# Kernel optimization log

Measured on AMD Instinct MI355X. Metric: run time of the kernel, lower is better.

Reference implementation:

```python
import jax, jax.numpy as jnp
import numpy as np

R = 16            # search_range
D = 2 * R + 1     # 33 offsets per axis -> 1089 cost channels
B, C, H, W = 64, 256, 16, 16
OUT = 512         # conv channels for search_range=16
FULLY = 1024
EPS_BN = 1e-5
EPS_NORM = 1e-12
LRELU_SLOPE = 0.01


def l2_normalize(x):
    # torch F.normalize(x, dim=1, p=2): x / clamp_min(||x||_2, 1e-12)
    n = jnp.sqrt(jnp.sum(x * x, axis=1, keepdims=True))
    return x / jnp.maximum(n, EPS_NORM)


def cost_volume(c1, warp, r):
    # Fused equivalent of the original (2r+1)^2 Python-loop of slice/mul/mean:
    # one dense correlation GEMM over the padded map, then a gather of the
    # diagonal-band entries. cost[b,dy,dx,i,j] = mean_c c1[b,c,i,j]*pad[b,c,i+dy,j+dx]
    b, c, h, w = c1.shape
    d = 2 * r + 1
    padded = jnp.pad(warp, ((0, 0), (0, 0), (r, r), (r, r)))          # (B,C,h+2r,w+2r)
    full = jnp.einsum('bcij,bcuv->bijuv', c1, padded) / c             # (B,h,w,h+2r,w+2r)
    dy = jnp.arange(d)
    ii = jnp.arange(h)
    jj = jnp.arange(w)
    I = ii[None, None, :, None]                 # (1,1,h,1)
    J = jj[None, None, None, :]                 # (1,1,1,w)
    U = dy[:, None, None, None] + I             # (d,1,h,1)
    V = dy[None, :, None, None] + J             # (1,d,1,w)
    cost = full[:, I, J, U, V]                  # (B,d,d,h,w)
    cost = cost.reshape(b, d * d, h, w)
    return jnp.where(cost > 0, cost, LRELU_SLOPE * cost)  # LeakyReLU(0.01)


def conv_bn_relu(x, Wc, bc, g, be, stride):
    y = jax.lax.conv_general_dilated(
        x, Wc, window_strides=(stride, stride), padding=((1, 1), (1, 1)),
        dimension_numbers=('NCHW', 'OIHW', 'NCHW'))
    y = y + bc[None, :, None, None]
    # training-mode BatchNorm: biased batch stats over (B,H,W)
    mu = jnp.mean(y, axis=(0, 2, 3), keepdims=True)
    var = jnp.var(y, axis=(0, 2, 3), keepdims=True)
    y = (y - mu) * jax.lax.rsqrt(var + EPS_BN)
    y = y * g[None, :, None, None] + be[None, :, None, None]
    return jnp.maximum(y, 0.0)


def setup_inputs() -> dict:
    key = jax.random.key(0)
    ks = jax.random.split(key, 10)
    s = 0.02
    inp = {
        'feature1': jax.random.normal(ks[0], (B, C, H, W), jnp.float32),
        'feature2': jax.random.normal(ks[1], (B, C, H, W), jnp.float32),
        'W1': jax.random.normal(ks[2], (OUT, D * D, 3, 3), jnp.float32) * s,
        'b1': jnp.zeros((OUT,), jnp.float32),
        'g1': jnp.ones((OUT,), jnp.float32),
        'be1': jnp.zeros((OUT,), jnp.float32),
        'W2': jax.random.normal(ks[3], (OUT, OUT, 3, 3), jnp.float32) * s,
        'b2': jnp.zeros((OUT,), jnp.float32),
        'g2': jnp.ones((OUT,), jnp.float32),
        'be2': jnp.zeros((OUT,), jnp.float32),
        'W3': jax.random.normal(ks[4], (OUT, OUT, 3, 3), jnp.float32) * s,
        'b3': jnp.zeros((OUT,), jnp.float32),
        'g3': jnp.ones((OUT,), jnp.float32),
        'be3': jnp.zeros((OUT,), jnp.float32),
        'Wf1': jax.random.normal(ks[5], (FULLY, 256 * OUT), jnp.float32) * s,
        'bf1': jnp.zeros((FULLY,), jnp.float32),
        'Wf2': jax.random.normal(ks[6], (8, FULLY), jnp.float32) * s,
        'bf2': jnp.zeros((8,), jnp.float32),
    }
    return inp


def reference(feature1, feature2, W1, b1, g1, be1, W2, b2, g2, be2,
              W3, b3, g3, be3, Wf1, bf1, Wf2, bf2):
    # warped=False: normalize both feature maps
    gc = cost_volume(l2_normalize(feature1), l2_normalize(feature2), R)
    x = conv_bn_relu(gc, W1, b1, g1, be1, 1)
    x = conv_bn_relu(x, W2, b2, g2, be2, 1)
    x = conv_bn_relu(x, W3, b3, g3, be3, 1)
    x = x.reshape(x.shape[0], -1)               # (B, 512*16*16)
    x = jnp.maximum(x @ Wf1.T + bf1, 0.0)       # Linear + ReLU
    # Dropout treated as identity (deterministic reference)
    offset = x @ Wf2.T + bf2                    # (B, 8)
    return offset
```

## Files before the change

### kernel.cpp

```cpp
#include <hip/hip_runtime.h>
#include <hip/hip_bf16.h>
#include <stdint.h>


typedef unsigned short ushort_t;
typedef __attribute__((ext_vector_type(8))) short     bf16x8;
typedef __attribute__((ext_vector_type(8))) unsigned short u16x8;
typedef __attribute__((ext_vector_type(4))) unsigned short u16x4;
typedef __attribute__((ext_vector_type(4))) float     f32x4;

#define NB   64
#define NC   256
#define NP   256
#define KCV  256
#define KP1  1152
#define NOUT 512
#define NROWS 16384
#define KFC  131072
#define NF   1024
#define KSPL 32

__device__ __forceinline__ unsigned short f2bf(float x) {
  union { float f; unsigned u; } c; c.f = x;
  unsigned r = c.u + 0x7FFFu + ((c.u >> 16) & 1u);
// ... 89 lines not shown
                  : (const ushort_t*)0;
  }

  for (int kc = 0; kc < KCV; kc += 64) {
#pragma unroll
    for (int s = 0; s < 4; ++s) {
      int idx = tid + (s << 8);
      gl_lds16(srcA[s] + kc, &As[idx * 8]);
      const ushort_t* g = srcB[s] ? srcB[s] + kc : zerot;
      gl_lds16(g, &Bs[idx * 8]);
    }
    __syncthreads();
#pragma unroll
    for (int kk = 0; kk < 2; ++kk) {
      bf16x8 af[4], bfv[4];
#pragma unroll
      for (int mi = 0; mi < 4; ++mi)
        af[mi] = *(const bf16x8*)&As[(wr * 64 + mi * 16 + la) * 64 + kk * 32 + lb * 8];
#pragma unroll
      for (int ni = 0; ni < 4; ++ni)
        bfv[ni] = *(const bf16x8*)&Bs[(wc * 64 + ni * 16 + la) * 64 + kk * 32 + lb * 8];
#pragma unroll
      for (int mi = 0; mi < 4; ++mi)
#pragma unroll
        for (int ni = 0; ni < 4; ++ni)
          acc[mi][ni] = mfma16(af[mi], bfv[ni], acc[mi][ni]);
    }
    __syncthreads();
  }

  const float sc = 1.f / 256.f;
#pragma unroll
  for (int ni = 0; ni < 4; ++ni) {
    int uv = n0 + wc * 64 + ni * 16 + la;
    int u = uv / 48, v = uv - u * 48;
#pragma unroll
    for (int mi = 0; mi < 4; ++mi) {
      int ij = m0 + wr * 64 + mi * 16 + lb * 4;
#pragma unroll
      for (int r = 0; r < 4; ++r) {
        int ijr = ij + r;
        int i = ijr >> 4, j = ijr & 15;
        int dy = u - i, dx = v - j;
        if ((unsigned)dy < 33u && (unsigned)dx < 33u) {
          float vv = acc[mi][ni][r] * sc;
          vv = vv > 0.f ? vv : 0.01f * vv;
          costT[((size_t)b * NP + ijr) * KP1 + dy * 33 + dx] = f2bf(vv);
        }
      }
    }
  }
}

__global__ __launch_bounds__(512, 1) void conv_gemm256(
    const ushort_t* __restrict__ X, const ushort_t* __restrict__ Wp,
    const float* __restrict__ bias, ushort_t* __restrict__ Y0,
    ushort_t* __restrict__ Y1, const int K, const int TPT, const int NT2,
    const ushort_t* __restrict__ zerot)
{
  __shared__ ushort_t lds[65536];
  const int tid = threadIdx.x;
  const int lane = tid & 63, wave = tid >> 6;
  const int wr = wave >> 2, wc = wave & 3;
  const int la = lane & 15, lb = lane >> 4;

  const int bid = blockIdx.x;
  const int L = ((bid & 7) << 5) + (bid >> 3);
  const int g = L >> 7;
  const int rem = L & 127;
  const int b = rem >> 1;
  const int n0 = (rem & 1) << 8;
  const int t0 = g * NT2;

  int amask[4];
  const ushort_t* abase[4];
  const ushort_t* bbase[4];
#pragma unroll
  for (int s = 0; s < 4; ++s) {
    int idx = tid + (s << 9);
    int ks = idx & 7, loc = (idx >> 3) & 63;
    int rA = ((s & 1) << 7) + ((s >> 1) << 6) + loc;
    int i = rA >> 4, j = rA & 15;
    int m = 0;
#pragma unroll
    for (int tap = 0; tap < 9; ++tap) {
      int i2 = i + tap / 3 - 1, j2 = j + tap % 3 - 1;
      if (((unsigned)i2 < 16u) & ((unsigned)j2 < 16u)) m |= 1 << tap;
    }
    amask[s] = m;
    abase[s] = X + (size_t)(b * NP + rA) * K + ((ks ^ (rA & 7)) << 3);
    int rB = ((s & 1) << 7) + ((loc >> 5) << 6) + ((s >> 1) << 5) + (loc & 31);
    bbase[s] = Wp + (size_t)(n0 + rB) * K + ((ks ^ (rB & 7)) << 3);
  }

  const int ck0 = ((0 + lb) ^ (la & 7)) << 3;
  const int ck1 = ((4 + lb) ^ (la & 7)) << 3;
  const int a_base = wr * 4096 + la * 64;
  const int b_base = 16384 + (wc >> 1) * 4096 + (wc & 1) * 2048 + la * 64;

  f32x4 acc[8][4];
#pragma unroll
  for (int i = 0; i < 8; ++i)
#pragma unroll
    for (int j = 0; j < 4; ++j) acc[i][j] = (f32x4){0.f, 0.f, 0.f, 0.f};

  auto tile_par = [&](int tg, int& toffA, size_t& wtap, int& tap) {
    tap = tg / TPT;
    int kc = (tg - tap * TPT) << 6;
    int ty = tap / 3;
    toffA = (ty * 16 + (tap - 3 * ty) - 17) * K + kc;
    wtap  = (size_t)tap * NOUT * K + kc;
  };

#define STAGE_A(S) { const ushort_t* gp = ((amask[S] >> tapN) & 1) ? abase[S] + toffN : zerot; \
                     gl_lds16(gp, &bufn[(tid + ((S) << 9)) * 8]); }
#define STAGE_B(S) gl_lds16(bbase[S] + wtapN, &bufn[16384 + (tid + ((S) << 9)) * 8]);

#define READ_A03() \
  Af[0][0] = *(const bf16x8*)&buf[a_base + 0    + ck0]; Af[0][1] = *(const bf16x8*)&buf[a_base + 0    + ck1]; \
  Af[1][0] = *(const bf16x8*)&buf[a_base + 1024 + ck0]; Af[1][1] = *(const bf16x8*)&buf[a_base + 1024 + ck1]; \
  Af[2][0] = *(const bf16x8*)&buf[a_base + 2048 + ck0]; Af[2][1] = *(const bf16x8*)&buf[a_base + 2048 + ck1]; \
  Af[3][0] = *(const bf16x8*)&buf[a_base + 3072 + ck0]; Af[3][1] = *(const bf16x8*)&buf[a_base + 3072 + ck1];
#define READ_A47() \
  Af[4][0] = *(const bf16x8*)&buf[a_base + 8192 + 0    + ck0]; Af[4][1] = *(const bf16x8*)&buf[a_base + 8192 + 0    + ck1]; \
  Af[5][0] = *(const bf16x8*)&buf[a_base + 8192 + 1024 + ck0]; Af[5][1] = *(const bf16x8*)&buf[a_base + 8192 + 1024 + ck1]; \
  Af[6][0] = *(const bf16x8*)&buf[a_base + 8192 + 2048 + ck0]; Af[6][1] = *(const bf16x8*)&buf[a_base + 8192 + 2048 + ck1]; \
  Af[7][0] = *(const bf16x8*)&buf[a_base + 8192 + 3072 + ck0]; Af[7][1] = *(const bf16x8*)&buf[a_base + 8192 + 3072 + ck1];
#define READ_B(NOFF) \
  bf00 = *(const bf16x8*)&buf[b_base + (NOFF) + 0    + ck0]; bf01 = *(const bf16x8*)&buf[b_base + (NOFF) + 0    + ck1]; \
  bf10 = *(const bf16x8*)&buf[b_base + (NOFF) + 1024 + ck0]; bf11 = *(const bf16x8*)&buf[b_base + (NOFF) + 1024 + ck1];
#define MFMA_QUAD(MB, N0, N1) \
  acc[MB+0][N0] = mfma16(Af[MB+0][0], bf00, acc[MB+0][N0]); \
  acc[MB+0][N1] = mfma16(Af[MB+0][0], bf10, acc[MB+0][N1]); \
  acc[MB+1][N0] = mfma16(Af[MB+1][0], bf00, acc[MB+1][N0]); \
  acc[MB+1][N1] = mfma16(Af[MB+1][0], bf10, acc[MB+1][N1]); \
  acc[MB+2][N0] = mfma16(Af[MB+2][0], bf00, acc[MB+2][N0]); \
  acc[MB+2][N1] = mfma16(Af[MB+2][0], bf10, acc[MB+2][N1]); \
  acc[MB+3][N0] = mfma16(Af[MB+3][0], bf00, acc[MB+3][N0]); \
  acc[MB+3][N1] = mfma16(Af[MB+3][0], bf10, acc[MB+3][N1]); \
  acc[MB+0][N0] = mfma16(Af[MB+0][1], bf01, acc[MB+0][N0]); \
  acc[MB+0][N1] = mfma16(Af[MB+0][1], bf11, acc[MB+0][N1]); \
  acc[MB+1][N0] = mfma16(Af[MB+1][1], bf01, acc[MB+1][N0]); \
  acc[MB+1][N1] = mfma16(Af[MB+1][1], bf11, acc[MB+1][N1]); \
  acc[MB+2][N0] = mfma16(Af[MB+2][1], bf01, acc[MB+2][N0]); \
  acc[MB+2][N1] = mfma16(Af[MB+2][1], bf11, acc[MB+2][N1]); \
  acc[MB+3][N0] = mfma16(Af[MB+3][1], bf01, acc[MB+3][N0]); \
  acc[MB+3][N1] = mfma16(Af[MB+3][1], bf11, acc[MB+3][N1]);

  {
    ushort_t* bufn = &lds[0];
    int tapN, toffN; size_t wtapN;
    tile_par(t0, toffN, wtapN, tapN);
    STAGE_A(0) STAGE_A(1) STAGE_A(2) STAGE_A(3)
    STAGE_B(0) STAGE_B(1) STAGE_B(2) STAGE_B(3)
  }
  asm volatile("s_waitcnt vmcnt(2)" ::: "memory");
  __builtin_amdgcn_s_barrier();

  bf16x8 Af[8][2];

  for (int t = 0; t < NT2 - 1; ++t) {
    const ushort_t* buf = &lds[(t & 1) << 15];
    ushort_t* bufn = &lds[((t + 1) & 1) << 15];
    int tapN, toffN; size_t wtapN;
    tile_par(t0 + t + 1, toffN, wtapN, tapN);
    bf16x8 bf00, bf01, bf10, bf11;

    READ_A03()
    READ_B(0)
    STAGE_A(0) STAGE_A(1)
    asm volatile("s_waitcnt vmcnt(6)" ::: "memory");
    __builtin_amdgcn_s_barrier();
    asm volatile("s_waitcnt lgkmcnt(0)" ::: "memory");
    __builtin_amdgcn_sched_barrier(0);
    __builtin_amdgcn_s_setprio(1);
    MFMA_QUAD(0, 0, 1)
    __builtin_amdgcn_s_setprio(0);

    READ_A47()
    READ_B(0)
    STAGE_A(2) STAGE_A(3)
    asm volatile("s_waitcnt vmcnt(4)" ::: "memory");
    __builtin_amdgcn_s_barrier();
    asm volatile("s_waitcnt lgkmcnt(0)" ::: "memory");
    __builtin_amdgcn_sched_barrier(0);
    __builtin_amdgcn_s_setprio(1);
    MFMA_QUAD(4, 0, 1)
    __builtin_amdgcn_s_setprio(0);

    READ_B(8192)
    STAGE_B(0) STAGE_B(1)
    __builtin_amdgcn_s_barrier();
    asm volatile("s_waitcnt lgkmcnt(0)" ::: "memory");
    __builtin_amdgcn_sched_barrier(0);
    __builtin_amdgcn_s_setprio(1);
    MFMA_QUAD(0, 2, 3)
    __builtin_amdgcn_s_setprio(0);

    READ_B(8192)
    STAGE_B(2) STAGE_B(3)
    asm volatile("s_waitcnt vmcnt(2)" ::: "memory");
    __builtin_amdgcn_s_barrier();
    asm volatile("s_waitcnt lgkmcnt(0)" ::: "memory");
    __builtin_amdgcn_sched_barrier(0);
    __builtin_amdgcn_s_setprio(1);
    MFMA_QUAD(4, 2, 3)
    __builtin_amdgcn_s_setprio(0);
  }

  {
    const ushort_t* buf = &lds[((NT2 - 1) & 1) << 15];
    bf16x8 bf00, bf01, bf10, bf11;
    asm volatile("s_waitcnt vmcnt(0)" ::: "memory");
    __builtin_amdgcn_s_barrier();
    READ_A03()
    READ_B(0)
    asm volatile("s_waitcnt lgkmcnt(0)" ::: "memory");
    __builtin_amdgcn_sched_barrier(0);
    MFMA_QUAD(0, 0, 1)
    READ_A47()
    asm volatile("s_waitcnt lgkmcnt(0)" ::: "memory");
    __builtin_amdgcn_sched_barrier(0);
    MFMA_QUAD(4, 0, 1)
    READ_B(8192)
    asm volatile("s_waitcnt lgkmcnt(0)" ::: "memory");
    __builtin_amdgcn_sched_barrier(0);
    MFMA_QUAD(0, 2, 3)
    MFMA_QUAD(4, 2, 3)
  }

  ushort_t* Yh = g ? Y1 : Y0;
#pragma unroll
  for (int ni = 0; ni < 4; ++ni) {
    int col = n0 + wc * 64 + ni * 16 + la;
    float bv = 0.5f * bias[col];
#pragma unroll
    for (int mi = 0; mi < 8; ++mi) {
      int row = b * NP + wr * 128 + mi * 16 + lb * 4;
#pragma unroll
      for (int r = 0; r < 4; ++r)
        Yh[(size_t)(row + r) * NOUT + col] = f2bf(acc[mi][ni][r] + bv);
    }
  }
#undef STAGE_A
#undef STAGE_B
#undef READ_A03
#undef READ_A47
#undef READ_B
#undef MFMA_QUAD
}

__global__ __launch_bounds__(512) void bn_stat2(
    const ushort_t* __restrict__ Y0, const ushort_t* __restrict__ Y1,
    float* __restrict__ st)
{
  const int col = threadIdx.x;
  const size_t base = (size_t)blockIdx.x * 32 * NOUT;
  float s = 0.f, q = 0.f;
  for (int r = 0; r < 32; ++r) {
    float y = b2f(Y0[base + r * NOUT + col]) + b2f(Y1[base + r * NOUT + col]);
    s += y; q += y * y;
  }
  atomicAdd(&st[col], s);
  atomicAdd(&st[512 + col], q);
}

__global__ __launch_bounds__(256) void bn_apply2(
    const ushort_t* __restrict__ Y0, const ushort_t* __restrict__ Y1,
    const float* __restrict__ st, const float* __restrict__ g,
    const float* __restrict__ be, ushort_t* __restrict__ Xo)
{
  const size_t idx = (size_t)blockIdx.x * 256 + threadIdx.x;
  u16x8 a = *(const u16x8*)(Y0 + idx * 8);
  u16x8 c = *(const u16x8*)(Y1 + idx * 8);
  const int c0 = (int)((idx * 8) & 511);
  u16x8 pk;
#pragma unroll
  for (int q = 0; q < 8; ++q) {
    int cc = c0 + q;
    float y = b2f(a[q]) + b2f(c[q]);
    float mu  = st[cc] * (1.f / 16384.f);
    float var = st[512 + cc] * (1.f / 16384.f) - mu * mu;
    float s = rsqrtf(var + 1e-5f) * g[cc];
    pk[q] = f2bf(fmaxf((y - mu) * s + be[cc], 0.f));
  }
  *(u16x8*)(Xo + idx * 8) = pk;
}

__global__ __launch_bounds__(256) void bn_apply2_t(
    const ushort_t* __restrict__ Y0, const ushort_t* __restrict__ Y1,
    const float* __restrict__ st, const float* __restrict__ g,
    const float* __restrict__ be, ushort_t* __restrict__ Xf)
{
  __shared__ ushort_t T[64][65];
  const int c0  = blockIdx.x * 64;
  const int ij0 = blockIdx.y * 64;
  const int b   = blockIdx.z;
  const int tid = threadIdx.x;

#pragma unroll
  for (int it = 0; it < 16; ++it) {
    int e = it * 256 + tid;
// ... 127 lines not shown
  const float* g2  = (const float*)d_in[8];
  const float* be2 = (const float*)d_in[9];
  const float* W3  = (const float*)d_in[10];
  const float* b3  = (const float*)d_in[11];
  const float* g3  = (const float*)d_in[12];
  const float* be3 = (const float*)d_in[13];
  const float* Wf1 = (const float*)d_in[14];
  const float* bf1 = (const float*)d_in[15];
  const float* Wf2 = (const float*)d_in[16];
  const float* bf2 = (const float*)d_in[17];
  float* out = (float*)d_out;

  char* ws = (char*)d_ws;
  size_t off = 0;
  auto alloc = [&](size_t bytes) -> void* {
    void* p = ws + off;
    off += (bytes + 255) & ~(size_t)255;
    return p;
  };

  ushort_t* zerot = (ushort_t*)alloc(256);
  float* st1  = (float*)alloc(1024 * 4);
  float* st2  = (float*)alloc(1024 * 4);
  float* st3  = (float*)alloc(1024 * 4);
  const size_t zero_bytes = off;

  float* hacc = (float*)alloc((size_t)KSPL * NB * NF * 4);
  const size_t SZ_AT   = (size_t)NB * NP * NC * 2;
  const size_t SZ_COST = (size_t)NB * NP * KP1 * 2;
  const size_t SZ_WP1  = (size_t)9 * NOUT * KP1 * 2;
  const size_t SZ_WP23 = (size_t)9 * NOUT * 512 * 2;
  ushort_t* AT    = (ushort_t*)alloc(SZ_AT);
  ushort_t* N2T   = (ushort_t*)alloc(SZ_AT);
  ushort_t* costT = (ushort_t*)alloc(SZ_COST);
  ushort_t* Wp1   = (ushort_t*)alloc(SZ_WP1);
  ushort_t* Wp2   = (ushort_t*)alloc(SZ_WP23);
  ushort_t* Wp3   = (ushort_t*)alloc(SZ_WP23);
  ushort_t* Yh0   = (ushort_t*)alloc((size_t)NROWS * NOUT * 2);
  ushort_t* Yh1   = (ushort_t*)alloc((size_t)NROWS * NOUT * 2);
  ushort_t* Xbuf  = (ushort_t*)alloc((size_t)NROWS * NOUT * 2);
  ushort_t* Xf    = (ushort_t*)alloc((size_t)NB * KFC * 2);

  hipMemsetAsync(ws, 0, zero_bytes, stream);
  hipMemsetAsync(costT, 0, SZ_COST, stream);

  l2norm_t<<<dim3(64, 2), 256, 0, stream>>>(f1, f2, AT, N2T);

  pack_w<<<(9 * NOUT * KP1 + 255) / 256, 256, 0, stream>>>(W1, Wp1, 1089, KP1, 9 * NOUT * KP1);
  pack_w<<<(9 * NOUT * 512 + 255) / 256, 256, 0, stream>>>(W2, Wp2, 512, 512, 9 * NOUT * 512);
  pack_w<<<(9 * NOUT * 512 + 255) / 256, 256, 0, stream>>>(W3, Wp3, 512, 512, 9 * NOUT * 512);

  cv_gemm<<<dim3(18, 2, 64), 256, 0, stream>>>(AT, N2T, costT, zerot);

  conv_gemm256<<<256, 512, 0, stream>>>(costT, Wp1, b1, Yh0, Yh1, KP1, 18, 81, zerot);
  bn_stat2<<<512, 512, 0, stream>>>(Yh0, Yh1, st1);
  bn_apply2<<<4096, 256, 0, stream>>>(Yh0, Yh1, st1, g1, be1, Xbuf);

  conv_gemm256<<<256, 512, 0, stream>>>(Xbuf, Wp2, b2, Yh0, Yh1, 512, 8, 36, zerot);
  bn_stat2<<<512, 512, 0, stream>>>(Yh0, Yh1, st2);
  bn_apply2<<<4096, 256, 0, stream>>>(Yh0, Yh1, st2, g2, be2, Xbuf);

  conv_gemm256<<<256, 512, 0, stream>>>(Xbuf, Wp3, b3, Yh0, Yh1, 512, 8, 36, zerot);
  bn_stat2<<<512, 512, 0, stream>>>(Yh0, Yh1, st3);
  bn_apply2_t<<<dim3(8, 4, 64), 256, 0, stream>>>(Yh0, Yh1, st3, g3, be3, Xf);

  fc1_gemm<<<dim3(16, KSPL), 256, 0, stream>>>(Xf, Wf1, hacc);
  fc2_out<<<64, 256, 0, stream>>>(hacc, bf1, Wf2, bf2, out);

  (void)in_sizes; (void)n_in; (void)out_size; (void)ws_size;
}
```

Before: 621.2 us.

## Reuse staged activation tile across all nine conv taps via shifted LDS reads

The implicit-GEMM conv kernel now loads each 256-row by 64-channel activation chunk into LDS once and reuses it for all nine 3x3 taps. It does this by reading LDS rows shifted by the tap offset, with out-of-bounds rows redirected to a zeroed LDS slot. Before, a masked, shifted copy of the activations was re-fetched from global memory for every tap. The aim is to cut global and L2 traffic for the A operand roughly ninefold. In exchange the weight tile is still streamed every tap, with only double buffering, and the schedule waits with vmcnt(0) after each tap, which may expose load latency.

```diff
diff --git a/kernel.cpp b/kernel.cpp
--- a/kernel.cpp
+++ b/kernel.cpp
@@ -165,13 +165,12 @@
   }
 }
 
-__global__ __launch_bounds__(512, 1) void conv_gemm256(
+__global__ __launch_bounds__(512, 1) void conv_tap(
     const ushort_t* __restrict__ X, const ushort_t* __restrict__ Wp,
     const float* __restrict__ bias, ushort_t* __restrict__ Y0,
-    ushort_t* __restrict__ Y1, const int K, const int TPT, const int NT2,
-    const ushort_t* __restrict__ zerot)
-{
-  __shared__ ushort_t lds[65536];
+    ushort_t* __restrict__ Y1, const int K, const int Kh, const int nc)
+{
+  __shared__ ushort_t lds[65600];
   const int tid = threadIdx.x;
   const int lane = tid & 63, wave = tid >> 6;
   const int wr = wave >> 2, wc = wave & 3;
@@ -183,33 +182,25 @@
   const int rem = L & 127;
   const int b = rem >> 1;
   const int n0 = (rem & 1) << 8;
-  const int t0 = g * NT2;
-
-  int amask[4];
+  const int koff0 = g * Kh;
+
+  if (tid < 8) *(u16x8*)&lds[65536 + tid * 8] = (u16x8){0,0,0,0,0,0,0,0};
+
   const ushort_t* abase[4];
   const ushort_t* bbase[4];
 #pragma unroll
   for (int s = 0; s < 4; ++s) {
     int idx = tid + (s << 9);
-    int ks = idx & 7, loc = (idx >> 3) & 63;
-    int rA = ((s & 1) << 7) + ((s >> 1) << 6) + loc;
-    int i = rA >> 4, j = rA & 15;
-    int m = 0;
-#pragma unroll
-    for (int tap = 0; tap < 9; ++tap) {
-      int i2 = i + tap / 3 - 1, j2 = j + tap % 3 - 1;
-      if (((unsigned)i2 < 16u) & ((unsigned)j2 < 16u)) m |= 1 << tap;
-    }
-    amask[s] = m;
-    abase[s] = X + (size_t)(b * NP + rA) * K + ((ks ^ (rA & 7)) << 3);
+    int row = idx >> 3, ck = idx & 7;
+    abase[s] = X + (size_t)(b * NP + row) * K + ((ck ^ (row & 7)) << 3);
+    int loc = (idx >> 3) & 63, ks = idx & 7;
     int rB = ((s & 1) << 7) + ((loc >> 5) << 6) + ((s >> 1) << 5) + (loc & 31);
     bbase[s] = Wp + (size_t)(n0 + rB) * K + ((ks ^ (rB & 7)) << 3);
   }
 
-  const int ck0 = ((0 + lb) ^ (la & 7)) << 3;
-  const int ck1 = ((4 + lb) ^ (la & 7)) << 3;
-  const int a_base = wr * 4096 + la * 64;
-  const int b_base = 16384 + (wc >> 1) * 4096 + (wc & 1) * 2048 + la * 64;
+  const int ckB0 = ((0 + lb) ^ (la & 7)) << 3;
+  const int ckB1 = ((4 + lb) ^ (la & 7)) << 3;
+  const int wread = (wc >> 1) * 4096 + (wc & 1) * 2048 + la * 64;
 
   f32x4 acc[8][4];
 #pragma unroll
@@ -217,129 +208,152 @@
 #pragma unroll
     for (int j = 0; j < 4; ++j) acc[i][j] = (f32x4){0.f, 0.f, 0.f, 0.f};
 
-  auto tile_par = [&](int tg, int& toffA, size_t& wtap, int& tap) {
-    tap = tg / TPT;
-    int kc = (tg - tap * TPT) << 6;
-    int ty = tap / 3;
-    toffA = (ty * 16 + (tap - 3 * ty) - 17) * K + kc;
-    wtap  = (size_t)tap * NOUT * K + kc;
-  };
-
-#define STAGE_A(S) { const ushort_t* gp = ((amask[S] >> tapN) & 1) ? abase[S] + toffN : zerot; \
-                     gl_lds16(gp, &bufn[(tid + ((S) << 9)) * 8]); }
-#define STAGE_B(S) gl_lds16(bbase[S] + wtapN, &bufn[16384 + (tid + ((S) << 9)) * 8]);
-
-#define READ_A03() \
-  Af[0][0] = *(const bf16x8*)&buf[a_base + 0    + ck0]; Af[0][1] = *(const bf16x8*)&buf[a_base + 0    + ck1]; \
-  Af[1][0] = *(const bf16x8*)&buf[a_base + 1024 + ck0]; Af[1][1] = *(const bf16x8*)&buf[a_base + 1024 + ck1]; \
-  Af[2][0] = *(const bf16x8*)&buf[a_base + 2048 + ck0]; Af[2][1] = *(const bf16x8*)&buf[a_base + 2048 + ck1]; \
-  Af[3][0] = *(const bf16x8*)&buf[a_base + 3072 + ck0]; Af[3][1] = *(const bf16x8*)&buf[a_base + 3072 + ck1];
-#define READ_A47() \
-  Af[4][0] = *(const bf16x8*)&buf[a_base + 8192 + 0    + ck0]; Af[4][1] = *(const bf16x8*)&buf[a_base + 8192 + 0    + ck1]; \
-  Af[5][0] = *(const bf16x8*)&buf[a_base + 8192 + 1024 + ck0]; Af[5][1] = *(const bf16x8*)&buf[a_base + 8192 + 1024 + ck1]; \
-  Af[6][0] = *(const bf16x8*)&buf[a_base + 8192 + 2048 + ck0]; Af[6][1] = *(const bf16x8*)&buf[a_base + 8192 + 2048 + ck1]; \
-  Af[7][0] = *(const bf16x8*)&buf[a_base + 8192 + 3072 + ck0]; Af[7][1] = *(const bf16x8*)&buf[a_base + 8192 + 3072 + ck1];
-#define READ_B(NOFF) \
-  bf00 = *(const bf16x8*)&buf[b_base + (NOFF) + 0    + ck0]; bf01 = *(const bf16x8*)&buf[b_base + (NOFF) + 0    + ck1]; \
-  bf10 = *(const bf16x8*)&buf[b_base + (NOFF) + 1024 + ck0]; bf11 = *(const bf16x8*)&buf[b_base + (NOFF) + 1024 + ck1];
-#define MFMA_QUAD(MB, N0, N1) \
-  acc[MB+0][N0] = mfma16(Af[MB+0][0], bf00, acc[MB+0][N0]); \
-  acc[MB+0][N1] = mfma16(Af[MB+0][0], bf10, acc[MB+0][N1]); \
-  acc[MB+1][N0] = mfma16(Af[MB+1][0], bf00, acc[MB+1][N0]); \
-  acc[MB+1][N1] = mfma16(Af[MB+1][0], bf10, acc[MB+1][N1]); \
-  acc[MB+2][N0] = mfma16(Af[MB+2][0], bf00, acc[MB+2][N0]); \
-  acc[MB+2][N1] = mfma16(Af[MB+2][0], bf10, acc[MB+2][N1]); \
-  acc[MB+3][N0] = mfma16(Af[MB+3][0], bf00, acc[MB+3][N0]); \
-  acc[MB+3][N1] = mfma16(Af[MB+3][0], bf10, acc[MB+3][N1]); \
-  acc[MB+0][N0] = mfma16(Af[MB+0][1], bf01, acc[MB+0][N0]); \
-  acc[MB+0][N1] = mfma16(Af[MB+0][1], bf11, acc[MB+0][N1]); \
-  acc[MB+1][N0] = mfma16(Af[MB+1][1], bf01, acc[MB+1][N0]); \
-  acc[MB+1][N1] = mfma16(Af[MB+1][1], bf11, acc[MB+1][N1]); \
-  acc[MB+2][N0] = mfma16(Af[MB+2][1], bf01, acc[MB+2][N0]); \
-  acc[MB+2][N1] = mfma16(Af[MB+2][1], bf11, acc[MB+2][N1]); \
-  acc[MB+3][N0] = mfma16(Af[MB+3][1], bf01, acc[MB+3][N0]); \
-  acc[MB+3][N1] = mfma16(Af[MB+3][1], bf11, acc[MB+3][N1]);
-
+  const int nsteps = nc * 9;
+
+#pragma unroll
+  for (int s = 0; s < 4; ++s)
+    gl_lds16(abase[s] + koff0, &lds[(tid + (s << 9)) * 8]);
   {
-    ushort_t* bufn = &lds[0];
-    int tapN, toffN; size_t wtapN;
-    tile_par(t0, toffN, wtapN, tapN);
-    STAGE_A(0) STAGE_A(1) STAGE_A(2) STAGE_A(3)
-    STAGE_B(0) STAGE_B(1) STAGE_B(2) STAGE_B(3)
-  }
-  asm volatile("s_waitcnt vmcnt(2)" ::: "memory");
+    size_t wko = (size_t)koff0;
+#pragma unroll
+    for (int s = 0; s < 4; ++s)
+      gl_lds16(bbase[s] + wko, &lds[32768 + (tid + (s << 9)) * 8]);
+  }
+  asm volatile("s_waitcnt vmcnt(0)" ::: "memory");
   __builtin_amdgcn_s_barrier();
 
-  bf16x8 Af[8][2];
-
-  for (int t = 0; t < NT2 - 1; ++t) {
-    const ushort_t* buf = &lds[(t & 1) << 15];
-    ushort_t* bufn = &lds[((t + 1) & 1) << 15];
-    int tapN, toffN; size_t wtapN;
-    tile_par(t0 + t + 1, toffN, wtapN, tapN);
-    bf16x8 bf00, bf01, bf10, bf11;
-
-    READ_A03()
-    READ_B(0)
-    STAGE_A(0) STAGE_A(1)
-    asm volatile("s_waitcnt vmcnt(6)" ::: "memory");
-    __builtin_amdgcn_s_barrier();
-    asm volatile("s_waitcnt lgkmcnt(0)" ::: "memory");
-    __builtin_amdgcn_sched_barrier(0);
-    __builtin_amdgcn_s_setprio(1);
-    MFMA_QUAD(0, 0, 1)
-    __builtin_amdgcn_s_setprio(0);
-
-    READ_A47()
-    READ_B(0)
-    STAGE_A(2) STAGE_A(3)
-    asm volatile("s_waitcnt vmcnt(4)" ::: "memory");
-    __builtin_amdgcn_s_barrier();
-    asm volatile("s_waitcnt lgkmcnt(0)" ::: "memory");
-    __builtin_amdgcn_sched_barrier(0);
-    __builtin_amdgcn_s_setprio(1);
-    MFMA_QUAD(4, 0, 1)
-    __builtin_amdgcn_s_setprio(0);
-
-    READ_B(8192)
-    STAGE_B(0) STAGE_B(1)
-    __builtin_amdgcn_s_barrier();
-    asm volatile("s_waitcnt lgkmcnt(0)" ::: "memory");
-    __builtin_amdgcn_sched_barrier(0);
-    __builtin_amdgcn_s_setprio(1);
-    MFMA_QUAD(0, 2, 3)
-    __builtin_amdgcn_s_setprio(0);
-
-    READ_B(8192)
-    STAGE_B(2) STAGE_B(3)
-    asm volatile("s_waitcnt vmcnt(2)" ::: "memory");
-    __builtin_amdgcn_s_barrier();
-    asm volatile("s_waitcnt lgkmcnt(0)" ::: "memory");
-    __builtin_amdgcn_sched_barrier(0);
-    __builtin_amdgcn_s_setprio(1);
-    MFMA_QUAD(4, 2, 3)
-    __builtin_amdgcn_s_setprio(0);
-  }
-
-  {
-    const ushort_t* buf = &lds[((NT2 - 1) & 1) << 15];
-    bf16x8 bf00, bf01, bf10, bf11;
-    asm volatile("s_waitcnt vmcnt(0)" ::: "memory");
-    __builtin_amdgcn_s_barrier();
-    READ_A03()
-    READ_B(0)
-    asm volatile("s_waitcnt lgkmcnt(0)" ::: "memory");
-    __builtin_amdgcn_sched_barrier(0);
-    MFMA_QUAD(0, 0, 1)
-    READ_A47()
-    asm volatile("s_waitcnt lgkmcnt(0)" ::: "memory");
-    __builtin_amdgcn_sched_barrier(0);
-    MFMA_QUAD(4, 0, 1)
-    READ_B(8192)
-    asm volatile("s_waitcnt lgkmcnt(0)" ::: "memory");
-    __builtin_amdgcn_sched_barrier(0);
-    MFMA_QUAD(0, 2, 3)
-    MFMA_QUAD(4, 2, 3)
+  for (int c = 0; c < nc; ++c) {
+    const int aC = (c & 1) << 14;
+    ushort_t* an = &lds[((c + 1) & 1) << 14];
+    for (int tap = 0; tap < 9; ++tap) {
+      const int step = c * 9 + tap;
+      const int wC = 32768 + ((step & 1) << 14);
+      ushort_t* wn = &lds[32768 + (((step + 1) & 1) << 14)];
+      const bool has_next = step < nsteps - 1;
+      const bool stageA = (tap == 7) && (c < nc - 1);
+      int tapN = (tap < 8) ? tap + 1 : 0;
+      int cN   = (tap < 8) ? c : c + 1;
+      size_t wkoN = (size_t)tapN * NOUT * K + koff0 + cN * 64;
+      int akoN = koff0 + (c + 1) * 64;
+
+      const int ty = tap / 3, tx = tap - 3 * ty;
+      const int dA = (ty - 1) * 16 + (tx - 1);
+      const int sx = (la + dA) & 7;
+      const int ckA0 = ((lb ^ sx) << 3);
+      const int ckA1 = (((4 + lb) ^ sx) << 3);
+      const int rbase = wr * 128 + la + dA;
+      const int ibase = wr * 8 + ty - 1;
+      const bool jok = !((tx == 0) & (la == 0)) & !((tx == 2) & (la == 15));
+
+      bf16x8 Af[4][2];
+      bf16x8 b01_00, b01_01, b01_10, b01_11;
+      bf16x8 b23_00, b23_01, b23_10, b23_11;
+
+#pragma unroll
+      for (int mi = 0; mi < 4; ++mi) {
+        bool ok = jok && ((unsigned)(ibase + mi) < 16u);
+        int r = (rbase + mi * 16) * 64;
+        int a0 = ok ? aC + r + ckA0 : 65536;
+        int a1 = ok ? aC + r + ckA1 : 65536;
+        Af[mi][0] = *(const bf16x8*)&lds[a0];
+        Af[mi][1] = *(const bf16x8*)&lds[a1];
+      }
+      b01_00 = *(const bf16x8*)&lds[wC + wread + 0    + ckB0];
+      b01_01 = *(const bf16x8*)&lds[wC + wread + 0    + ckB1];
+      b01_10 = *(const bf16x8*)&lds[wC + wread + 1024 + ckB0];
+      b01_11 = *(const bf16x8*)&lds[wC + wread + 1024 + ckB1];
+      if (has_next) {
+        gl_lds16(bbase[0] + wkoN, &wn[(tid + 0 * 512) * 8]);
+        gl_lds16(bbase[1] + wkoN, &wn[(tid + 1 * 512) * 8]);
+      }
+      asm volatile("s_waitcnt lgkmcnt(0)" ::: "memory");
+      __builtin_amdgcn_sched_barrier(0);
+      __builtin_amdgcn_s_setprio(1);
+#pragma unroll
+      for (int mi = 0; mi < 4; ++mi) {
+        acc[mi][0] = mfma16(Af[mi][0], b01_00, acc[mi][0]);
+        acc[mi][1] = mfma16(Af[mi][0], b01_10, acc[mi][1]);
+      }
+#pragma unroll
+      for (int mi = 0; mi < 4; ++mi) {
+        acc[mi][0] = mfma16(Af[mi][1], b01_01, acc[mi][0]);
+        acc[mi][1] = mfma16(Af[mi][1], b01_11, acc[mi][1]);
+      }
+      __builtin_amdgcn_s_setprio(0);
+
+      b23_00 = *(const bf16x8*)&lds[wC + 8192 + wread + 0    + ckB0];
+      b23_01 = *(const bf16x8*)&lds[wC + 8192 + wread + 0    + ckB1];
+      b23_10 = *(const bf16x8*)&lds[wC + 8192 + wread + 1024 + ckB0];
+      b23_11 = *(const bf16x8*)&lds[wC + 8192 + wread + 1024 + ckB1];
+      if (has_next) {
+        gl_lds16(bbase[2] + wkoN, &wn[(tid + 2 * 512) * 8]);
+        gl_lds16(bbase[3] + wkoN, &wn[(tid + 3 * 512) * 8]);
+      }
+      if (stageA) {
+        gl_lds16(abase[0] + akoN, &an[(tid + 0 * 512) * 8]);
+        gl_lds16(abase[1] + akoN, &an[(tid + 1 * 512) * 8]);
+      }
+      asm volatile("s_waitcnt lgkmcnt(0)" ::: "memory");
+      __builtin_amdgcn_sched_barrier(0);
+      __builtin_amdgcn_s_setprio(1);
+#pragma unroll
+      for (int mi = 0; mi < 4; ++mi) {
+        acc[mi][2] = mfma16(Af[mi][0], b23_00, acc[mi][2]);
+        acc[mi][3] = mfma16(Af[mi][0], b23_10, acc[mi][3]);
+      }
+#pragma unroll
+      for (int mi = 0; mi < 4; ++mi) {
+        acc[mi][2] = mfma16(Af[mi][1], b23_01, acc[mi][2]);
+        acc[mi][3] = mfma16(Af[mi][1], b23_11, acc[mi][3]);
+      }
+      __builtin_amdgcn_s_setprio(0);
+
+#pragma unroll
+      for (int mi = 0; mi < 4; ++mi) {
+        bool ok = jok && ((unsigned)(ibase + 4 + mi) < 16u);
+        int r = (rbase + (4 + mi) * 16) * 64;
+        int a0 = ok ? aC + r + ckA0 : 65536;
+        int a1 = ok ? aC + r + ckA1 : 65536;
+        Af[mi][0] = *(const bf16x8*)&lds[a0];
+        Af[mi][1] = *(const bf16x8*)&lds[a1];
+      }
+      if (stageA) {
+        gl_lds16(abase[2] + akoN, &an[(tid + 2 * 512) * 8]);
+        gl_lds16(abase[3] + akoN, &an[(tid + 3 * 512) * 8]);
+      }
+      asm volatile("s_waitcnt lgkmcnt(0)" ::: "memory");
+      __builtin_amdgcn_sched_barrier(0);
+      __builtin_amdgcn_s_setprio(1);
+#pragma unroll
+      for (int mi = 0; mi < 4; ++mi) {
+        acc[4 + mi][0] = mfma16(Af[mi][0], b01_00, acc[4 + mi][0]);
+        acc[4 + mi][1] = mfma16(Af[mi][0], b01_10, acc[4 + mi][1]);
+      }
+#pragma unroll
+      for (int mi = 0; mi < 4; ++mi) {
+        acc[4 + mi][0] = mfma16(Af[mi][1], b01_01, acc[4 + mi][0]);
+        acc[4 + mi][1] = mfma16(Af[mi][1], b01_11, acc[4 + mi][1]);
+      }
+      __builtin_amdgcn_s_setprio(0);
+
+      __builtin_amdgcn_s_setprio(1);
+#pragma unroll
+      for (int mi = 0; mi < 4; ++mi) {
+        acc[4 + mi][2] = mfma16(Af[mi][0], b23_00, acc[4 + mi][2]);
+        acc[4 + mi][3] = mfma16(Af[mi][0], b23_10, acc[4 + mi][3]);
+      }
+#pragma unroll
+      for (int mi = 0; mi < 4; ++mi) {
+        acc[4 + mi][2] = mfma16(Af[mi][1], b23_01, acc[4 + mi][2]);
+        acc[4 + mi][3] = mfma16(Af[mi][1], b23_11, acc[4 + mi][3]);
+      }
+      __builtin_amdgcn_s_setprio(0);
+      if (has_next) {
+        if (stageA) asm volatile("s_waitcnt vmcnt(4)" ::: "memory");
+        else        asm volatile("s_waitcnt vmcnt(0)" ::: "memory");
+      }
+      __builtin_amdgcn_s_barrier();
+    }
   }
 
   ushort_t* Yh = g ? Y1 : Y0;
@@ -355,12 +369,6 @@
         Yh[(size_t)(row + r) * NOUT + col] = f2bf(acc[mi][ni][r] + bv);
     }
   }
-#undef STAGE_A
-#undef STAGE_B
-#undef READ_A03
-#undef READ_A47
-#undef READ_B
-#undef MFMA_QUAD
 }
 
 __global__ __launch_bounds__(512) void bn_stat2(
@@ -594,15 +602,15 @@
 
   cv_gemm<<<dim3(18, 2, 64), 256, 0, stream>>>(AT, N2T, costT, zerot);
 
-  conv_gemm256<<<256, 512, 0, stream>>>(costT, Wp1, b1, Yh0, Yh1, KP1, 18, 81, zerot);
+  conv_tap<<<256, 512, 0, stream>>>(costT, Wp1, b1, Yh0, Yh1, KP1, 576, 9);
   bn_stat2<<<512, 512, 0, stream>>>(Yh0, Yh1, st1);
   bn_apply2<<<4096, 256, 0, stream>>>(Yh0, Yh1, st1, g1, be1, Xbuf);
 
-  conv_gemm256<<<256, 512, 0, stream>>>(Xbuf, Wp2, b2, Yh0, Yh1, 512, 8, 36, zerot);
+  conv_tap<<<256, 512, 0, stream>>>(Xbuf, Wp2, b2, Yh0, Yh1, 512, 256, 4);
   bn_stat2<<<512, 512, 0, stream>>>(Yh0, Yh1, st2);
   bn_apply2<<<4096, 256, 0, stream>>>(Yh0, Yh1, st2, g2, be2, Xbuf);
 
-  conv_gemm256<<<256, 512, 0, stream>>>(Xbuf, Wp3, b3, Yh0, Yh1, 512, 8, 36, zerot);
+  conv_tap<<<256, 512, 0, stream>>>(Xbuf, Wp3, b3, Yh0, Yh1, 512, 256, 4);
   bn_stat2<<<512, 512, 0, stream>>>(Yh0, Yh1, st3);
   bn_apply2_t<<<dim3(8, 4, 64), 256, 0, stream>>>(Yh0, Yh1, st3, g3, be3, Xf);
 
```

After: 622.1 us. Within noise of the previous version (+0.1%).

## Restructure conv GEMM into 8-phase ping-pong pipeline with channel-split K

Applied to the files above, without the earlier changes.

Rewrites the conv GEMM main loop into an 8-phase schedule that processes two K tiles per iteration. Each phase issues LDS reads plus part of the next tile's global-to-LDS staging, then runs 16 MFMAs between barriers. The split-K partition across the two output halves now divides the channel range instead of the flat tile range. Conv1 is padded to an even tile count, and out-of-range taps load from a zero tile. This adds extra barriers per phase and a full vmcnt(0) wait each half-iteration, which can stall the pipeline.

```diff
diff --git a/kernel.cpp b/kernel.cpp
--- a/kernel.cpp
+++ b/kernel.cpp
@@ -165,10 +165,10 @@
   }
 }
 
-__global__ __launch_bounds__(512, 1) void conv_gemm256(
+__global__ __launch_bounds__(512, 1) void conv8p(
     const ushort_t* __restrict__ X, const ushort_t* __restrict__ Wp,
     const float* __restrict__ bias, ushort_t* __restrict__ Y0,
-    ushort_t* __restrict__ Y1, const int K, const int TPT, const int NT2,
+    ushort_t* __restrict__ Y1, const int K, const int TPT, const int NT,
     const ushort_t* __restrict__ zerot)
 {
   __shared__ ushort_t lds[65536];
@@ -183,7 +183,7 @@
   const int rem = L & 127;
   const int b = rem >> 1;
   const int n0 = (rem & 1) << 8;
-  const int t0 = g * NT2;
+  const int koff0 = g * (TPT << 6);
 
   int amask[4];
   const ushort_t* abase[4];
@@ -191,9 +191,8 @@
 #pragma unroll
   for (int s = 0; s < 4; ++s) {
     int idx = tid + (s << 9);
-    int ks = idx & 7, loc = (idx >> 3) & 63;
-    int rA = ((s & 1) << 7) + ((s >> 1) << 6) + loc;
-    int i = rA >> 4, j = rA & 15;
+    int row = idx >> 3, ck = idx & 7;
+    int i = row >> 4, j = row & 15;
     int m = 0;
 #pragma unroll
     for (int tap = 0; tap < 9; ++tap) {
@@ -201,15 +200,14 @@
       if (((unsigned)i2 < 16u) & ((unsigned)j2 < 16u)) m |= 1 << tap;
     }
     amask[s] = m;
-    abase[s] = X + (size_t)(b * NP + rA) * K + ((ks ^ (rA & 7)) << 3);
-    int rB = ((s & 1) << 7) + ((loc >> 5) << 6) + ((s >> 1) << 5) + (loc & 31);
-    bbase[s] = Wp + (size_t)(n0 + rB) * K + ((ks ^ (rB & 7)) << 3);
-  }
-
-  const int ck0 = ((0 + lb) ^ (la & 7)) << 3;
-  const int ck1 = ((4 + lb) ^ (la & 7)) << 3;
-  const int a_base = wr * 4096 + la * 64;
-  const int b_base = 16384 + (wc >> 1) * 4096 + (wc & 1) * 2048 + la * 64;
+    abase[s] = X + (size_t)(b * NP + row) * K + ((ck ^ (row & 7)) << 3);
+    bbase[s] = Wp + (size_t)(n0 + row) * K + ((ck ^ (row & 7)) << 3);
+  }
+
+  const int ck0 = ((lb ^ (la & 7)) << 3);
+  const int ck1 = (((4 + lb) ^ (la & 7)) << 3);
+  const int arow = (wr * 128 + la) * 64;
+  const int brow = 16384 + (wc * 64 + la) * 64;
 
   f32x4 acc[8][4];
 #pragma unroll
@@ -217,129 +215,137 @@
 #pragma unroll
     for (int j = 0; j < 4; ++j) acc[i][j] = (f32x4){0.f, 0.f, 0.f, 0.f};
 
-  auto tile_par = [&](int tg, int& toffA, size_t& wtap, int& tap) {
-    tap = tg / TPT;
-    int kc = (tg - tap * TPT) << 6;
+  auto tpar = [&](int t, int& tap, int& toffA, size_t& wtap) {
+    tap = t / TPT;
+    int kc = koff0 + ((t - tap * TPT) << 6);
     int ty = tap / 3;
     toffA = (ty * 16 + (tap - 3 * ty) - 17) * K + kc;
     wtap  = (size_t)tap * NOUT * K + kc;
   };
 
-#define STAGE_A(S) { const ushort_t* gp = ((amask[S] >> tapN) & 1) ? abase[S] + toffN : zerot; \
-                     gl_lds16(gp, &bufn[(tid + ((S) << 9)) * 8]); }
-#define STAGE_B(S) gl_lds16(bbase[S] + wtapN, &bufn[16384 + (tid + ((S) << 9)) * 8]);
-
-#define READ_A03() \
-  Af[0][0] = *(const bf16x8*)&buf[a_base + 0    + ck0]; Af[0][1] = *(const bf16x8*)&buf[a_base + 0    + ck1]; \
-  Af[1][0] = *(const bf16x8*)&buf[a_base + 1024 + ck0]; Af[1][1] = *(const bf16x8*)&buf[a_base + 1024 + ck1]; \
-  Af[2][0] = *(const bf16x8*)&buf[a_base + 2048 + ck0]; Af[2][1] = *(const bf16x8*)&buf[a_base + 2048 + ck1]; \
-  Af[3][0] = *(const bf16x8*)&buf[a_base + 3072 + ck0]; Af[3][1] = *(const bf16x8*)&buf[a_base + 3072 + ck1];
-#define READ_A47() \
-  Af[4][0] = *(const bf16x8*)&buf[a_base + 8192 + 0    + ck0]; Af[4][1] = *(const bf16x8*)&buf[a_base + 8192 + 0    + ck1]; \
-  Af[5][0] = *(const bf16x8*)&buf[a_base + 8192 + 1024 + ck0]; Af[5][1] = *(const bf16x8*)&buf[a_base + 8192 + 1024 + ck1]; \
-  Af[6][0] = *(const bf16x8*)&buf[a_base + 8192 + 2048 + ck0]; Af[6][1] = *(const bf16x8*)&buf[a_base + 8192 + 2048 + ck1]; \
-  Af[7][0] = *(const bf16x8*)&buf[a_base + 8192 + 3072 + ck0]; Af[7][1] = *(const bf16x8*)&buf[a_base + 8192 + 3072 + ck1];
-#define READ_B(NOFF) \
-  bf00 = *(const bf16x8*)&buf[b_base + (NOFF) + 0    + ck0]; bf01 = *(const bf16x8*)&buf[b_base + (NOFF) + 0    + ck1]; \
-  bf10 = *(const bf16x8*)&buf[b_base + (NOFF) + 1024 + ck0]; bf11 = *(const bf16x8*)&buf[b_base + (NOFF) + 1024 + ck1];
-#define MFMA_QUAD(MB, N0, N1) \
-  acc[MB+0][N0] = mfma16(Af[MB+0][0], bf00, acc[MB+0][N0]); \
-  acc[MB+0][N1] = mfma16(Af[MB+0][0], bf10, acc[MB+0][N1]); \
-  acc[MB+1][N0] = mfma16(Af[MB+1][0], bf00, acc[MB+1][N0]); \
-  acc[MB+1][N1] = mfma16(Af[MB+1][0], bf10, acc[MB+1][N1]); \
-  acc[MB+2][N0] = mfma16(Af[MB+2][0], bf00, acc[MB+2][N0]); \
-  acc[MB+2][N1] = mfma16(Af[MB+2][0], bf10, acc[MB+2][N1]); \
-  acc[MB+3][N0] = mfma16(Af[MB+3][0], bf00, acc[MB+3][N0]); \
-  acc[MB+3][N1] = mfma16(Af[MB+3][0], bf10, acc[MB+3][N1]); \
-  acc[MB+0][N0] = mfma16(Af[MB+0][1], bf01, acc[MB+0][N0]); \
-  acc[MB+0][N1] = mfma16(Af[MB+0][1], bf11, acc[MB+0][N1]); \
-  acc[MB+1][N0] = mfma16(Af[MB+1][1], bf01, acc[MB+1][N0]); \
-  acc[MB+1][N1] = mfma16(Af[MB+1][1], bf11, acc[MB+1][N1]); \
-  acc[MB+2][N0] = mfma16(Af[MB+2][1], bf01, acc[MB+2][N0]); \
-  acc[MB+2][N1] = mfma16(Af[MB+2][1], bf11, acc[MB+2][N1]); \
-  acc[MB+3][N0] = mfma16(Af[MB+3][1], bf01, acc[MB+3][N0]); \
-  acc[MB+3][N1] = mfma16(Af[MB+3][1], bf11, acc[MB+3][N1]);
+#define STAGE_A(S, BUFN, TAPN, TOFFN) { \
+  const ushort_t* gp = ((amask[S] >> (TAPN)) & 1) ? abase[S] + (TOFFN) : zerot; \
+  gl_lds16(gp, &(BUFN)[(tid + ((S) << 9)) * 8]); }
+#define STAGE_B(S, BUFN, TAPN, WTAPN) { \
+  const ushort_t* gp = ((TAPN) < 9) ? bbase[S] + (WTAPN) : zerot; \
+  gl_lds16(gp, &(BUFN)[16384 + (tid + ((S) << 9)) * 8]); }
+
+#define READ_A(MH, BUF) \
+  Af[0][0] = *(const bf16x8*)&(BUF)[arow + (MH)*4096 + 0    + ck0]; \
+  Af[0][1] = *(const bf16x8*)&(BUF)[arow + (MH)*4096 + 0    + ck1]; \
+  Af[1][0] = *(const bf16x8*)&(BUF)[arow + (MH)*4096 + 1024 + ck0]; \
+  Af[1][1] = *(const bf16x8*)&(BUF)[arow + (MH)*4096 + 1024 + ck1]; \
+  Af[2][0] = *(const bf16x8*)&(BUF)[arow + (MH)*4096 + 2048 + ck0]; \
+  Af[2][1] = *(const bf16x8*)&(BUF)[arow + (MH)*4096 + 2048 + ck1]; \
+  Af[3][0] = *(const bf16x8*)&(BUF)[arow + (MH)*4096 + 3072 + ck0]; \
+  Af[3][1] = *(const bf16x8*)&(BUF)[arow + (MH)*4096 + 3072 + ck1];
+#define READ_B(NH, BUF) \
+  Bf[0][0] = *(const bf16x8*)&(BUF)[brow + (NH)*2048 + 0    + ck0]; \
+  Bf[0][1] = *(const bf16x8*)&(BUF)[brow + (NH)*2048 + 0    + ck1]; \
+  Bf[1][0] = *(const bf16x8*)&(BUF)[brow + (NH)*2048 + 1024 + ck0]; \
+  Bf[1][1] = *(const bf16x8*)&(BUF)[brow + (NH)*2048 + 1024 + ck1];
+#define MFMA16(MH, NH) \
+  acc[(MH)*4+0][(NH)*2+0] = mfma16(Af[0][0], Bf[0][0], acc[(MH)*4+0][(NH)*2+0]); \
+  acc[(MH)*4+0][(NH)*2+1] = mfma16(Af[0][0], Bf[1][0], acc[(MH)*4+0][(NH)*2+1]); \
+  acc[(MH)*4+1][(NH)*2+0] = mfma16(Af[1][0], Bf[0][0], acc[(MH)*4+1][(NH)*2+0]); \
+  acc[(MH)*4+1][(NH)*2+1] = mfma16(Af[1][0], Bf[1][0], acc[(MH)*4+1][(NH)*2+1]); \
+  acc[(MH)*4+2][(NH)*2+0] = mfma16(Af[2][0], Bf[0][0], acc[(MH)*4+2][(NH)*2+0]); \
+  acc[(MH)*4+2][(NH)*2+1] = mfma16(Af[2][0], Bf[1][0], acc[(MH)*4+2][(NH)*2+1]); \
+  acc[(MH)*4+3][(NH)*2+0] = mfma16(Af[3][0], Bf[0][0], acc[(MH)*4+3][(NH)*2+0]); \
+  acc[(MH)*4+3][(NH)*2+1] = mfma16(Af[3][0], Bf[1][0], acc[(MH)*4+3][(NH)*2+1]); \
+  acc[(MH)*4+0][(NH)*2+0] = mfma16(Af[0][1], Bf[0][1], acc[(MH)*4+0][(NH)*2+0]); \
+  acc[(MH)*4+0][(NH)*2+1] = mfma16(Af[0][1], Bf[1][1], acc[(MH)*4+0][(NH)*2+1]); \
+  acc[(MH)*4+1][(NH)*2+0] = mfma16(Af[1][1], Bf[0][1], acc[(MH)*4+1][(NH)*2+0]); \
+  acc[(MH)*4+1][(NH)*2+1] = mfma16(Af[1][1], Bf[1][1], acc[(MH)*4+1][(NH)*2+1]); \
+  acc[(MH)*4+2][(NH)*2+0] = mfma16(Af[2][1], Bf[0][1], acc[(MH)*4+2][(NH)*2+0]); \
+  acc[(MH)*4+2][(NH)*2+1] = mfma16(Af[2][1], Bf[1][1], acc[(MH)*4+2][(NH)*2+1]); \
+  acc[(MH)*4+3][(NH)*2+0] = mfma16(Af[3][1], Bf[0][1], acc[(MH)*4+3][(NH)*2+0]); \
+  acc[(MH)*4+3][(NH)*2+1] = mfma16(Af[3][1], Bf[1][1], acc[(MH)*4+3][(NH)*2+1]);
+
+#define PHASE_SYNC_PRE() \
+  __builtin_amdgcn_s_barrier(); \
+  asm volatile("s_waitcnt lgkmcnt(0)" ::: "memory"); \
+  __builtin_amdgcn_sched_barrier(0); \
+  __builtin_amdgcn_s_setprio(1);
+#define PHASE_SYNC_POST() \
+  __builtin_amdgcn_s_setprio(0); \
+  __builtin_amdgcn_s_barrier();
 
   {
+    int tap0, toff0; size_t wtap0;
+    tpar(0, tap0, toff0, wtap0);
     ushort_t* bufn = &lds[0];
-    int tapN, toffN; size_t wtapN;
-    tile_par(t0, toffN, wtapN, tapN);
-    STAGE_A(0) STAGE_A(1) STAGE_A(2) STAGE_A(3)
-    STAGE_B(0) STAGE_B(1) STAGE_B(2) STAGE_B(3)
-  }
-  asm volatile("s_waitcnt vmcnt(2)" ::: "memory");
+    STAGE_A(0, bufn, tap0, toff0) STAGE_A(1, bufn, tap0, toff0)
+    STAGE_A(2, bufn, tap0, toff0) STAGE_A(3, bufn, tap0, toff0)
+    STAGE_B(0, bufn, tap0, wtap0) STAGE_B(1, bufn, tap0, wtap0)
+    STAGE_B(2, bufn, tap0, wtap0) STAGE_B(3, bufn, tap0, wtap0)
+  }
+  asm volatile("s_waitcnt vmcnt(0)" ::: "memory");
   __builtin_amdgcn_s_barrier();
 
-  bf16x8 Af[8][2];
-
-  for (int t = 0; t < NT2 - 1; ++t) {
-    const ushort_t* buf = &lds[(t & 1) << 15];
-    ushort_t* bufn = &lds[((t + 1) & 1) << 15];
-    int tapN, toffN; size_t wtapN;
-    tile_par(t0 + t + 1, toffN, wtapN, tapN);
-    bf16x8 bf00, bf01, bf10, bf11;
-
-    READ_A03()
-    READ_B(0)
-    STAGE_A(0) STAGE_A(1)
-    asm volatile("s_waitcnt vmcnt(6)" ::: "memory");
-    __builtin_amdgcn_s_barrier();
-    asm volatile("s_waitcnt lgkmcnt(0)" ::: "memory");
-    __builtin_amdgcn_sched_barrier(0);
-    __builtin_amdgcn_s_setprio(1);
-    MFMA_QUAD(0, 0, 1)
-    __builtin_amdgcn_s_setprio(0);
-
-    READ_A47()
-    READ_B(0)
-    STAGE_A(2) STAGE_A(3)
-    asm volatile("s_waitcnt vmcnt(4)" ::: "memory");
-    __builtin_amdgcn_s_barrier();
-    asm volatile("s_waitcnt lgkmcnt(0)" ::: "memory");
-    __builtin_amdgcn_sched_barrier(0);
-    __builtin_amdgcn_s_setprio(1);
-    MFMA_QUAD(4, 0, 1)
-    __builtin_amdgcn_s_setprio(0);
-
-    READ_B(8192)
-    STAGE_B(0) STAGE_B(1)
-    __builtin_amdgcn_s_barrier();
-    asm volatile("s_waitcnt lgkmcnt(0)" ::: "memory");
-    __builtin_amdgcn_sched_barrier(0);
-    __builtin_amdgcn_s_setprio(1);
-    MFMA_QUAD(0, 2, 3)
-    __builtin_amdgcn_s_setprio(0);
-
-    READ_B(8192)
-    STAGE_B(2) STAGE_B(3)
-    asm volatile("s_waitcnt vmcnt(2)" ::: "memory");
-    __builtin_amdgcn_s_barrier();
-    asm volatile("s_waitcnt lgkmcnt(0)" ::: "memory");
-    __builtin_amdgcn_sched_barrier(0);
-    __builtin_amdgcn_s_setprio(1);
-    MFMA_QUAD(4, 2, 3)
-    __builtin_amdgcn_s_setprio(0);
-  }
-
-  {
-    const ushort_t* buf = &lds[((NT2 - 1) & 1) << 15];
-    bf16x8 bf00, bf01, bf10, bf11;
+  const ushort_t* bufA = &lds[0];
+  const ushort_t* bufB = &lds[32768];
+  ushort_t* stA = &lds[32768];
+  ushort_t* stC = &lds[0];
+
+  const int niter = NT >> 1;
+  for (int it = 0; it < niter; ++it) {
+    const int t0 = it << 1;
+    int tapB, toffB; size_t wtapB;
+    tpar(t0 + 1, tapB, toffB, wtapB);
+    int tapC = 0, toffC = 0; size_t wtapC = 0;
+    const bool sC = (t0 + 2) < NT;
+    if (sC) tpar(t0 + 2, tapC, toffC, wtapC);
+
+    bf16x8 Af[4][2], Bf[2][2];
+
+    READ_A(0, bufA)
+    READ_B(0, bufA)
+    STAGE_A(0, stA, tapB, toffB) STAGE_A(1, stA, tapB, toffB)
+    STAGE_A(2, stA, tapB, toffB) STAGE_A(3, stA, tapB, toffB)
+    PHASE_SYNC_PRE()
+    MFMA16(0, 0)
+    PHASE_SYNC_POST()
+    READ_B(1, bufA)
+    STAGE_B(0, stA, tapB, wtapB) STAGE_B(1, stA, tapB, wtapB)
+    PHASE_SYNC_PRE()
+    MFMA16(0, 1)
+    PHASE_SYNC_POST()
+    READ_A(1, bufA)
+    STAGE_B(2, stA, tapB, wtapB) STAGE_B(3, stA, tapB, wtapB)
+    PHASE_SYNC_PRE()
+    MFMA16(1, 1)
+    PHASE_SYNC_POST()
+    READ_B(0, bufA)
     asm volatile("s_waitcnt vmcnt(0)" ::: "memory");
-    __builtin_amdgcn_s_barrier();
-    READ_A03()
-    READ_B(0)
-    asm volatile("s_waitcnt lgkmcnt(0)" ::: "memory");
-    __builtin_amdgcn_sched_barrier(0);
-    MFMA_QUAD(0, 0, 1)
-    READ_A47()
-    asm volatile("s_waitcnt lgkmcnt(0)" ::: "memory");
-    __builtin_amdgcn_sched_barrier(0);
-    MFMA_QUAD(4, 0, 1)
-    READ_B(8192)
-    asm volatile("s_waitcnt lgkmcnt(0)" ::: "memory");
-    __builtin_amdgcn_sched_barrier(0);
-    MFMA_QUAD(0, 2, 3)
-    MFMA_QUAD(4, 2, 3)
+    PHASE_SYNC_PRE()
+    MFMA16(1, 0)
+    PHASE_SYNC_POST()
+
+    READ_A(0, bufB)
+    READ_B(0, bufB)
+    if (sC) {
+      STAGE_A(0, stC, tapC, toffC) STAGE_A(1, stC, tapC, toffC)
+      STAGE_A(2, stC, tapC, toffC) STAGE_A(3, stC, tapC, toffC)
+    }
+    PHASE_SYNC_PRE()
+    MFMA16(0, 0)
+    PHASE_SYNC_POST()
+    READ_B(1, bufB)
+    if (sC) { STAGE_B(0, stC, tapC, wtapC) STAGE_B(1, stC, tapC, wtapC) }
+    PHASE_SYNC_PRE()
+    MFMA16(0, 1)
+    PHASE_SYNC_POST()
+    READ_A(1, bufB)
+    if (sC) { STAGE_B(2, stC, tapC, wtapC) STAGE_B(3, stC, tapC, wtapC) }
+    PHASE_SYNC_PRE()
+    MFMA16(1, 1)
+    PHASE_SYNC_POST()
+    READ_B(0, bufB)
+    asm volatile("s_waitcnt vmcnt(0)" ::: "memory");
+    PHASE_SYNC_PRE()
+    MFMA16(1, 0)
+    PHASE_SYNC_POST()
   }
 
   ushort_t* Yh = g ? Y1 : Y0;
@@ -357,10 +363,11 @@
   }
 #undef STAGE_A
 #undef STAGE_B
-#undef READ_A03
-#undef READ_A47
+#undef READ_A
 #undef READ_B
-#undef MFMA_QUAD
+#undef MFMA16
+#undef PHASE_SYNC_PRE
+#undef PHASE_SYNC_POST
 }
 
 __global__ __launch_bounds__(512) void bn_stat2(
@@ -594,15 +601,15 @@
 
   cv_gemm<<<dim3(18, 2, 64), 256, 0, stream>>>(AT, N2T, costT, zerot);
 
-  conv_gemm256<<<256, 512, 0, stream>>>(costT, Wp1, b1, Yh0, Yh1, KP1, 18, 81, zerot);
+  conv8p<<<256, 512, 0, stream>>>(costT, Wp1, b1, Yh0, Yh1, KP1, 9, 82, zerot);
   bn_stat2<<<512, 512, 0, stream>>>(Yh0, Yh1, st1);
   bn_apply2<<<4096, 256, 0, stream>>>(Yh0, Yh1, st1, g1, be1, Xbuf);
 
-  conv_gemm256<<<256, 512, 0, stream>>>(Xbuf, Wp2, b2, Yh0, Yh1, 512, 8, 36, zerot);
+  conv8p<<<256, 512, 0, stream>>>(Xbuf, Wp2, b2, Yh0, Yh1, 512, 4, 36, zerot);
   bn_stat2<<<512, 512, 0, stream>>>(Yh0, Yh1, st2);
   bn_apply2<<<4096, 256, 0, stream>>>(Yh0, Yh1, st2, g2, be2, Xbuf);
 
-  conv_gemm256<<<256, 512, 0, stream>>>(Xbuf, Wp3, b3, Yh0, Yh1, 512, 8, 36, zerot);
+  conv8p<<<256, 512, 0, stream>>>(Xbuf, Wp3, b3, Yh0, Yh1, 512, 4, 36, zerot);
   bn_stat2<<<512, 512, 0, stream>>>(Yh0, Yh1, st3);
   bn_apply2_t<<<dim3(8, 4, 64), 256, 0, stream>>>(Yh0, Yh1, st3, g3, be3, Xf);
 
```

New measurement: 669.9 us. 1.08x slower.
